# Optimization experiments

Measured on AMD Instinct MI355X. Metric: run time of the kernel, lower is better.

Reference implementation:

```python
import jax, jax.numpy as jnp
import numpy as np

B, D_IN, D_EMB = 8192, 256, 128
N_EX, N_DUR = 16384, 64
N_TRAIN = 100000
THRESH = 1.0


def setup_inputs() -> dict:
    key = jax.random.key(0)
    ks = jax.random.split(key, 6)
    x = jax.random.normal(ks[0], (B, D_IN), jnp.float32)
    # small scales so pairwise distances straddle the threshold (realistic kernel regime)
    W = jax.random.normal(ks[1], (D_IN, D_EMB), jnp.float32) * 0.003
    b = jnp.zeros((D_EMB,), jnp.float32)
    E = jax.random.normal(ks[2], (N_EX, D_EMB), jnp.float32) * 0.05
    log_ev = jax.random.normal(ks[3], (N_EX, N_DUR), jnp.float32)
    log_cen = jax.random.normal(ks[4], (N_EX, N_DUR), jnp.float32)
    logit_h = jax.random.normal(ks[5], (N_DUR,), jnp.float32) - 3.0
    return {
        "input": x, "W": W, "b": b, "exemplar_embeddings": E,
        "log_exemplar_event_counts": log_ev,
        "log_exemplar_censor_counts": log_cen,
        "logit_baseline_hazard": logit_h,
    }


def _kernel_weights(x, W, b, E):
    # encoder (no_grad in original): single linear layer
    phi = x @ W + b  # [B, D_EMB]
    # cdist via Gram expansion; clamp tiny negatives from roundoff
    d2 = (jnp.sum(phi * phi, axis=1, keepdims=True)
          + jnp.sum(E * E, axis=1)[None, :]
          - 2.0 * (phi @ E.T))
    d2 = jnp.maximum(d2, 0.0)          # [B, N_EX] squared distances
    d = jnp.sqrt(d2)
    # threshold mask + exp kernel (matches exp(-distance**2))
    return jnp.where(d <= THRESH, jnp.exp(-d2), 0.0)


def reference(input, W, b, exemplar_embeddings,
              log_exemplar_event_counts, log_exemplar_censor_counts,
              logit_baseline_hazard):
    kw = jax.lax.stop_gradient(
        _kernel_weights(input, W, b, exemplar_embeddings))  # [B, N_EX]

    baseline_hazard = jax.nn.sigmoid(logit_baseline_hazard)  # [N_DUR]
    baseline_KM = jnp.exp(jnp.cumsum(jnp.log(1.0 - baseline_hazard + 1e-7)))

    ev = jnp.exp(log_exemplar_event_counts)    # [N_EX, N_DUR]
    cen = jnp.exp(log_exemplar_censor_counts)  # [N_EX, N_DUR]
    # reverse cumulative sum along durations = flip/cumsum/flip
    at_risk = jnp.flip(jnp.cumsum(jnp.flip(ev + cen, axis=1), axis=1), axis=1)
    pos = at_risk > 0
    hazards = jnp.where(pos, ev / jnp.where(pos, at_risk, 1.0), 0.0)
    exemplar_KM = jnp.exp(jnp.cumsum(jnp.log(1.0 - hazards + 1e-7), axis=1))

    gamma_n = jnp.exp(-(THRESH ** 2)) / N_TRAIN
    numer = kw @ exemplar_KM + gamma_n * baseline_KM[None, :]  # [B, N_DUR]
    denom = (jnp.sum(kw, axis=1) + gamma_n + 1e-12)[:, None]
    return jnp.clip(numer / denom, 1e-12, 1.0 - 1e-12)
```

## Files before the change

### kernel.cpp

```cpp
#include <hip/hip_runtime.h>

using short8  = __attribute__((ext_vector_type(8))) short;
using floatx4 = __attribute__((ext_vector_type(4))) float;

#define NB   8192
#define DIN  256
#define DE   128
#define NEX  16384
#define ND   64
#define ESPLIT 16
#define EPB  (NEX/ESPLIT)
#define TE   64
#define NTIL (EPB/TE)
#define GAMMA_N 3.6787944117144233e-06f

__device__ __forceinline__ unsigned short f2bf(float f) {
  unsigned int u = __float_as_uint(f);
  u += 0x7fffu + ((u >> 16) & 1u);
  return (unsigned short)(u >> 16);
}
__device__ __forceinline__ float bf2f(unsigned short h) {
  return __uint_as_float(((unsigned int)h) << 16);
}

__device__ __forceinline__ void gload_lds16(const void* g, void* l) {
  __builtin_amdgcn_global_load_lds(
      (const __attribute__((address_space(1))) void*)g,
      (__attribute__((address_space(3))) void*)l, 16, 0, 0);
}

__device__ __forceinline__ floatx4 mfma_bf16(short8 a, short8 b, floatx4 c) {
  return __builtin_amdgcn_mfma_f32_16x16x32_bf16(a, b, c, 0, 0, 0);
}

__global__ __launch_bounds__(256) void k_encoder(
    const float* __restrict__ x, const float* __restrict__ W,
    const float* __restrict__ bias, unsigned short* __restrict__ phi_bf,
    float* __restrict__ pn)
{
  __shared__ float xs[32 * DIN];
  __shared__ float part[32][2];
  const int rb  = blockIdx.x * 32;
  const int tid = threadIdx.x;
  for (int i = tid; i < 32 * DIN; i += 256) xs[i] = x[rb * DIN + i];
  __syncthreads();
  const int j  = tid & 127;
  const int rh = tid >> 7;
  const float bj = bias[j];
  float acc[16];
  #pragma unroll
  for (int r = 0; r < 16; ++r) acc[r] = bj;
  for (int k = 0; k < DIN; ++k) {
    const float wv = W[k * DE + j];
    #pragma unroll
    for (int r = 0; r < 16; ++r)
      acc[r] = fmaf(xs[(rh * 16 + r) * DIN + k], wv, acc[r]);
  }
  const int lane = tid & 63;
  const int jh   = (tid >> 6) & 1;
  #pragma unroll
  for (int r = 0; r < 16; ++r) {
    const int row = rh * 16 + r;
    const unsigned short hb = f2bf(acc[r]);
    phi_bf[(rb + row) * DE + j] = hb;
    const float hf = bf2f(hb);
    float sq = hf * hf;
    #pragma unroll
    for (int off = 1; off < 64; off <<= 1) sq += __shfl_xor(sq, off, 64);
    if (lane == 0) part[row][jh] = sq;
  }
  __syncthreads();
  if (tid < 32) pn[rb + tid] = part[tid][0] + part[tid][1];
}

__global__ __launch_bounds__(128) void k_prep_e(
    const float* __restrict__ E, unsigned short* __restrict__ E_bf,
    float* __restrict__ en)
{
  __shared__ float part[2];
  const int e = blockIdx.x;
  const int j = threadIdx.x;
  const unsigned short hb = f2bf(E[e * DE + j]);
  E_bf[e * DE + j] = hb;
  const float hf = bf2f(hb);
  float sq = hf * hf;
  #pragma unroll
  for (int off = 1; off < 64; off <<= 1) sq += __shfl_xor(sq, off, 64);
  if ((j & 63) == 0) part[j >> 6] = sq;
  __syncthreads();
  if (j == 0) en[e] = part[0] + part[1];
}

__global__ __launch_bounds__(256) void k_prep_km(
    const float* __restrict__ lev, const float* __restrict__ lcen,
    const float* __restrict__ lh, unsigned short* __restrict__ KM_t,
    float* __restrict__ baseKM)
{
  __shared__ unsigned short sm[64][65];
  const int tid = threadIdx.x;
  const int t   = tid & 63;
  const int wv  = tid >> 6;
  for (int ee = 0; ee < 16; ++ee) {
    const int el = wv * 16 + ee;
    const int e  = blockIdx.x * 64 + el;
    const float ev = __expf(lev[e * ND + t]);
    const float cn = __expf(lcen[e * ND + t]);
    float s = ev + cn;
    #pragma unroll
    for (int off = 1; off < 64; off <<= 1) {
      const float o = __shfl(s, (t + off) & 63, 64);
      s += (t + off < 64) ? o : 0.0f;
    }
    const float haz = (s > 0.0f) ? (ev / s) : 0.0f;
    float lc = __logf(1.0f - haz + 1e-7f);
    #pragma unroll
    for (int off = 1; off < 64; off <<= 1) {
      const float o = __shfl(lc, (t - off) & 63, 64);
      lc += (t >= off) ? o : 0.0f;
    }
    sm[el][t] = f2bf(__expf(lc));
  }
  __syncthreads();
  const int t_out = tid >> 2, prt = tid & 3;
  unsigned short tmp[16];
  #pragma unroll
  for (int i = 0; i < 16; ++i) tmp[i] = sm[prt * 16 + i][t_out];
  *reinterpret_cast<short8*>(KM_t + (size_t)t_out * NEX + blockIdx.x * 64 + prt * 16) =
      *reinterpret_cast<short8*>(&tmp[0]);
  *reinterpret_cast<short8*>(KM_t + (size_t)t_out * NEX + blockIdx.x * 64 + prt * 16 + 8) =
      *reinterpret_cast<short8*>(&tmp[8]);
  if (blockIdx.x == 0 && tid < 64) {
    const float h = 1.0f / (1.0f + __expf(-lh[t]));
    float l2 = __logf(1.0f - h + 1e-7f);
    #pragma unroll
    for (int off = 1; off < 64; off <<= 1) {
      const float o = __shfl(l2, (t - off) & 63, 64);
      l2 += (t >= off) ? o : 0.0f;
    }
    baseKM[t] = __expf(l2);
  }
}

__global__ __launch_bounds__(256, 4) void k_fused(
    const unsigned short* __restrict__ phi_bf, const float* __restrict__ pn,
    const unsigned short* __restrict__ E_bf, const float* __restrict__ en,
    const unsigned short* __restrict__ KM_t,
    float* __restrict__ numer_p, float* __restrict__ denom_p)
{
  __shared__ __align__(16) unsigned char E_lds[16384];
  __shared__ __align__(16) unsigned char KM_lds[8192];
  __shared__ __align__(16) unsigned char kw_lds[16384];

  const int tid = threadIdx.x;
  const int w   = tid >> 6;
  const int l   = tid & 63;
  const int lr  = l & 15;
  const int g   = l >> 4;
  const int rowbase = blockIdx.y * 128 + w * 32;
  const int ebase0  = blockIdx.x * EPB;
  const int swz = (lr & 7) << 4;

  short8 phiB[2][4];
  float  pnf[2];
  #pragma unroll
  for (int n = 0; n < 2; ++n) {
    const int r = rowbase + n * 16 + lr;
    #pragma unroll
    for (int kq = 0; kq < 4; ++kq)
      phiB[n][kq] = *reinterpret_cast<const short8*>(phi_bf + r * DE + kq * 32 + g * 8);
    pnf[n] = pn[r];
  }

  floatx4 c2[4][2];
  #pragma unroll
  for (int m2 = 0; m2 < 4; ++m2)
    #pragma unroll
    for (int n = 0; n < 2; ++n) c2[m2][n] = (floatx4){0.f, 0.f, 0.f, 0.f};
  float dn[2] = {0.f, 0.f};

  for (int it = 0; it < NTIL; ++it) {
    const int ebase = ebase0 + it * TE;
    __syncthreads();
    #pragma unroll
    for (int i = 0; i < 4; ++i) {
      const int c    = w * 4 + i;
      const int row  = c * 4 + (l >> 4);
      const int colB = (l & 15) * 16;
      gload_lds16((const char*)E_bf + (size_t)(ebase + row) * 256 +
                      (colB ^ ((row & 7) << 4)),
                  &E_lds[c * 1024]);
    }
    #pragma unroll
    for (int i = 0; i < 2; ++i) {
      const int c    = w * 2 + i;
      const int trow = c * 8 + (l >> 3);
      const int colB = (l & 7) * 16;
      gload_lds16((const char*)KM_t + (size_t)trow * (NEX * 2) + ebase * 2 +
                      (colB ^ ((trow & 7) << 4)),
                  &KM_lds[c * 1024]);
    }
    __syncthreads();

    #pragma unroll
    for (int m = 0; m < 4; ++m) {
      short8 ea[4];
      #pragma unroll
      for (int kq = 0; kq < 4; ++kq)
        ea[kq] = *reinterpret_cast<const short8*>(
            &E_lds[(m * 16 + lr) * 256 + ((kq * 64 + g * 16) ^ swz)]);
      floatx4 c1[2];
      c1[0] = (floatx4){0.f, 0.f, 0.f, 0.f};
      c1[1] = (floatx4){0.f, 0.f, 0.f, 0.f};
      #pragma unroll
      for (int kq = 0; kq < 4; ++kq) {
        c1[0] = mfma_bf16(ea[kq], phiB[0][kq], c1[0]);
        c1[1] = mfma_bf16(ea[kq], phiB[1][kq], c1[1]);
      }
      const floatx4 en4 = *reinterpret_cast<const floatx4*>(&en[ebase + m * 16 + g * 4]);
      #pragma unroll
      for (int n = 0; n < 2; ++n) {
        float kwv[4];
        #pragma unroll
        for (int rg = 0; rg < 4; ++rg) {
          float d2 = en4[rg] + pnf[n] - 2.0f * c1[n][rg];
          d2 = fmaxf(d2, 0.0f);
          kwv[rg] = (d2 <= 1.0f) ? __expf(-d2) : 0.0f;
          dn[n] += kwv[rg];
        }
        unsigned int pk0, pk1;
        asm("v_cvt_pk_bf16_f32 %0, %1, %2" : "=v"(pk0) : "v"(kwv[0]), "v"(kwv[1]));
        asm("v_cvt_pk_bf16_f32 %0, %1, %2" : "=v"(pk1) : "v"(kwv[2]), "v"(kwv[3]));
        const unsigned long long pk = (unsigned long long)pk0 |
                                      ((unsigned long long)pk1 << 32);
        *reinterpret_cast<unsigned long long*>(
            &kw_lds[w * 4096 + (n * 16 + lr) * 128 + ((m * 32 + g * 8) ^ swz)]) = pk;
      }
    }

    #pragma unroll
    for (int ks = 0; ks < 2; ++ks) {
      short8 kwB[2];
      #pragma unroll
      for (int n = 0; n < 2; ++n)
        kwB[n] = *reinterpret_cast<const short8*>(
            &kw_lds[w * 4096 + (n * 16 + lr) * 128 + ((ks * 64 + g * 16) ^ swz)]);
      #pragma unroll
      for (int m2 = 0; m2 < 4; ++m2) {
        const short8 kma = *reinterpret_cast<const short8*>(
            &KM_lds[(m2 * 16 + lr) * 128 + ((ks * 64 + g * 16) ^ swz)]);
        c2[m2][0] = mfma_bf16(kma, kwB[0], c2[m2][0]);
        c2[m2][1] = mfma_bf16(kma, kwB[1], c2[m2][1]);
      }
    }
  }

  #pragma unroll
  for (int n = 0; n < 2; ++n) {
    float v = dn[n];
    v += __shfl_xor(v, 16, 64);
    v += __shfl_xor(v, 32, 64);
    if (l < 16) denom_p[(size_t)blockIdx.x * NB + rowbase + n * 16 + lr] = v;
  }
  float* np = numer_p + ((size_t)blockIdx.x * NB + rowbase) * ND;
  #pragma unroll
  for (int n = 0; n < 2; ++n)
    #pragma unroll
    for (int m2 = 0; m2 < 4; ++m2)
      *reinterpret_cast<floatx4*>(&np[(n * 16 + lr) * ND + m2 * 16 + g * 4]) =
          c2[m2][n];
}

__global__ __launch_bounds__(256) void k_finalize(
    const float* __restrict__ numer_p, const float* __restrict__ denom_p,
    const float* __restrict__ baseKM, float* __restrict__ out)
{
  const int idx = blockIdx.x * 256 + threadIdx.x;
  const int b = idx >> 6;
  const int t = idx & 63;
  float num = 0.f, den = 0.f;
  #pragma unroll
  for (int s = 0; s < ESPLIT; ++s) {
    num += numer_p[(size_t)s * NB * ND + idx];
    den += denom_p[(size_t)s * NB + b];
  }
  num += GAMMA_N * baseKM[t];
  den += GAMMA_N + 1e-12f;
  float r = num / den;
  r = fminf(fmaxf(r, 1e-12f), 1.0f - 1e-12f);
  out[idx] = r;
}

extern "C" void kernel_launch(void* const* d_in, const int* in_sizes, int n_in,
                              void* d_out, int out_size, void* d_ws, size_t ws_size,
                              hipStream_t stream)
{
  const float* x    = (const float*)d_in[0];
  const float* W    = (const float*)d_in[1];
  const float* bias = (const float*)d_in[2];
  const float* E    = (const float*)d_in[3];
  const float* lev  = (const float*)d_in[4];
  const float* lcen = (const float*)d_in[5];
  const float* lh   = (const float*)d_in[6];
  float* out = (float*)d_out;

  char* ws = (char*)d_ws;
  size_t off = 0;
  auto alloc = [&](size_t bytes) -> void* {
    void* p = ws + off;
    off += (bytes + 255) & ~(size_t)255;
    return p;
  };
  unsigned short* phi_bf = (unsigned short*)alloc((size_t)NB * DE * 2);
  unsigned short* E_bf   = (unsigned short*)alloc((size_t)NEX * DE * 2);
  unsigned short* KM_t   = (unsigned short*)alloc((size_t)ND * NEX * 2);
  float* pn      = (float*)alloc((size_t)NB * 4);
  float* en      = (float*)alloc((size_t)NEX * 4);
  float* baseKM  = (float*)alloc((size_t)ND * 4);
  float* numer_p = (float*)alloc((size_t)ESPLIT * NB * ND * 4);
  float* denom_p = (float*)alloc((size_t)ESPLIT * NB * 4);

  k_encoder<<<NB / 32, 256, 0, stream>>>(x, W, bias, phi_bf, pn);
  k_prep_e<<<NEX, 128, 0, stream>>>(E, E_bf, en);
  k_prep_km<<<NEX / 64, 256, 0, stream>>>(lev, lcen, lh, KM_t, baseKM);
  k_fused<<<dim3(ESPLIT, NB / 128), 256, 0, stream>>>(phi_bf, pn, E_bf, en, KM_t,
                                                      numer_p, denom_p);
  k_finalize<<<(NB * ND) / 256, 256, 0, stream>>>(numer_p, denom_p, baseKM, out);
}
```

Baseline: 201.3 us.

## Vectorize prep kernels, halve kw LDS tile, store bf16 partials, double E split

```diff
diff --git a/kernel.cpp b/kernel.cpp
--- a/kernel.cpp
+++ b/kernel.cpp
@@ -8,7 +8,7 @@
 #define DE   128
 #define NEX  16384
 #define ND   64
-#define ESPLIT 16
+#define ESPLIT 32
 #define EPB  (NEX/ESPLIT)
 #define TE   64
 #define NTIL (EPB/TE)
@@ -22,6 +22,11 @@
 __device__ __forceinline__ float bf2f(unsigned short h) {
   return __uint_as_float(((unsigned int)h) << 16);
 }
+__device__ __forceinline__ unsigned int pk_bf16(float a, float b) {
+  unsigned int r;
+  asm("v_cvt_pk_bf16_f32 %0, %1, %2" : "=v"(r) : "v"(a), "v"(b));
+  return r;
+}
 
 __device__ __forceinline__ void gload_lds16(const void* g, void* l) {
   __builtin_amdgcn_global_load_lds(
@@ -39,56 +44,78 @@
     float* __restrict__ pn)
 {
   __shared__ float xs[32 * DIN];
-  __shared__ float part[32][2];
   const int rb  = blockIdx.x * 32;
   const int tid = threadIdx.x;
-  for (int i = tid; i < 32 * DIN; i += 256) xs[i] = x[rb * DIN + i];
+  for (int i = tid; i < 32 * DIN / 4; i += 256)
+    reinterpret_cast<float4*>(xs)[i] =
+        reinterpret_cast<const float4*>(x + (size_t)rb * DIN)[i];
   __syncthreads();
-  const int j  = tid & 127;
-  const int rh = tid >> 7;
-  const float bj = bias[j];
-  float acc[16];
-  #pragma unroll
-  for (int r = 0; r < 16; ++r) acc[r] = bj;
+  const int jt = tid & 31;
+  const int rt = tid >> 5;
+  const float4 bj = *reinterpret_cast<const float4*>(&bias[jt * 4]);
+  float4 a0 = bj, a1 = bj, a2 = bj, a3 = bj;
+  const float* xr = xs + rt * 4 * DIN;
+  #pragma unroll 4
   for (int k = 0; k < DIN; ++k) {
-    const float wv = W[k * DE + j];
-    #pragma unroll
-    for (int r = 0; r < 16; ++r)
-      acc[r] = fmaf(xs[(rh * 16 + r) * DIN + k], wv, acc[r]);
-  }
-  const int lane = tid & 63;
-  const int jh   = (tid >> 6) & 1;
-  #pragma unroll
-  for (int r = 0; r < 16; ++r) {
-    const int row = rh * 16 + r;
-    const unsigned short hb = f2bf(acc[r]);
-    phi_bf[(rb + row) * DE + j] = hb;
-    const float hf = bf2f(hb);
-    float sq = hf * hf;
-    #pragma unroll
-    for (int off = 1; off < 64; off <<= 1) sq += __shfl_xor(sq, off, 64);
-    if (lane == 0) part[row][jh] = sq;
-  }
-  __syncthreads();
-  if (tid < 32) pn[rb + tid] = part[tid][0] + part[tid][1];
-}
-
-__global__ __launch_bounds__(128) void k_prep_e(
+    const float4 wv = *reinterpret_cast<const float4*>(&W[k * DE + jt * 4]);
+    const float x0 = xr[k], x1 = xr[DIN + k], x2 = xr[2 * DIN + k], x3 = xr[3 * DIN + k];
+    a0.x = fmaf(x0, wv.x, a0.x); a0.y = fmaf(x0, wv.y, a0.y);
+    a0.z = fmaf(x0, wv.z, a0.z); a0.w = fmaf(x0, wv.w, a0.w);
+    a1.x = fmaf(x1, wv.x, a1.x); a1.y = fmaf(x1, wv.y, a1.y);
+    a1.z = fmaf(x1, wv.z, a1.z); a1.w = fmaf(x1, wv.w, a1.w);
+    a2.x = fmaf(x2, wv.x, a2.x); a2.y = fmaf(x2, wv.y, a2.y);
+    a2.z = fmaf(x2, wv.z, a2.z); a2.w = fmaf(x2, wv.w, a2.w);
+    a3.x = fmaf(x3, wv.x, a3.x); a3.y = fmaf(x3, wv.y, a3.y);
+    a3.z = fmaf(x3, wv.z, a3.z); a3.w = fmaf(x3, wv.w, a3.w);
+  }
+  float4 av[4] = {a0, a1, a2, a3};
+  #pragma unroll
+  for (int rr = 0; rr < 4; ++rr) {
+    const int row = rb + rt * 4 + rr;
+    const unsigned int p0 = pk_bf16(av[rr].x, av[rr].y);
+    const unsigned int p1 = pk_bf16(av[rr].z, av[rr].w);
+    *reinterpret_cast<uint2*>(phi_bf + (size_t)row * DE + jt * 4) =
+        make_uint2(p0, p1);
+    const float h0 = bf2f(p0 & 0xffff), h1 = bf2f(p0 >> 16);
+    const float h2 = bf2f(p1 & 0xffff), h3 = bf2f(p1 >> 16);
+    float s = h0 * h0 + h1 * h1 + h2 * h2 + h3 * h3;
+    s += __shfl_xor(s, 1, 64);
+    s += __shfl_xor(s, 2, 64);
+    s += __shfl_xor(s, 4, 64);
+    s += __shfl_xor(s, 8, 64);
+    s += __shfl_xor(s, 16, 64);
+    if (jt == 0) pn[row] = s;
+  }
+}
+
+__global__ __launch_bounds__(256) void k_prep_e(
     const float* __restrict__ E, unsigned short* __restrict__ E_bf,
     float* __restrict__ en)
 {
-  __shared__ float part[2];
-  const int e = blockIdx.x;
-  const int j = threadIdx.x;
-  const unsigned short hb = f2bf(E[e * DE + j]);
-  E_bf[e * DE + j] = hb;
-  const float hf = bf2f(hb);
-  float sq = hf * hf;
-  #pragma unroll
-  for (int off = 1; off < 64; off <<= 1) sq += __shfl_xor(sq, off, 64);
-  if ((j & 63) == 0) part[j >> 6] = sq;
-  __syncthreads();
-  if (j == 0) en[e] = part[0] + part[1];
+  const int tid = threadIdx.x;
+  const int w = tid >> 6, l = tid & 63;
+  const int row = blockIdx.x * 32 + w * 8 + (l >> 3);
+  const int c0  = (l & 7) * 16;
+  const float4* src = reinterpret_cast<const float4*>(E + (size_t)row * DE + c0);
+  float4 v0 = src[0], v1 = src[1], v2 = src[2], v3 = src[3];
+  unsigned int p[8];
+  p[0] = pk_bf16(v0.x, v0.y); p[1] = pk_bf16(v0.z, v0.w);
+  p[2] = pk_bf16(v1.x, v1.y); p[3] = pk_bf16(v1.z, v1.w);
+  p[4] = pk_bf16(v2.x, v2.y); p[5] = pk_bf16(v2.z, v2.w);
+  p[6] = pk_bf16(v3.x, v3.y); p[7] = pk_bf16(v3.z, v3.w);
+  uint4* dst = reinterpret_cast<uint4*>(E_bf + (size_t)row * DE + c0);
+  dst[0] = make_uint4(p[0], p[1], p[2], p[3]);
+  dst[1] = make_uint4(p[4], p[5], p[6], p[7]);
+  float s = 0.f;
+  #pragma unroll
+  for (int i = 0; i < 8; ++i) {
+    const float lo = bf2f(p[i] & 0xffff), hi = bf2f(p[i] >> 16);
+    s = fmaf(lo, lo, s); s = fmaf(hi, hi, s);
+  }
+  s += __shfl_xor(s, 1, 64);
+  s += __shfl_xor(s, 2, 64);
+  s += __shfl_xor(s, 4, 64);
+  if ((l & 7) == 0) en[row] = s;
 }
 
 __global__ __launch_bounds__(256) void k_prep_km(
@@ -141,15 +168,15 @@
   }
 }
 
-__global__ __launch_bounds__(256, 4) void k_fused(
+__global__ __launch_bounds__(256, 5) void k_fused(
     const unsigned short* __restrict__ phi_bf, const float* __restrict__ pn,
     const unsigned short* __restrict__ E_bf, const float* __restrict__ en,
     const unsigned short* __restrict__ KM_t,
-    float* __restrict__ numer_p, float* __restrict__ denom_p)
+    unsigned short* __restrict__ numer_p, float* __restrict__ denom_p)
 {
   __shared__ __align__(16) unsigned char E_lds[16384];
   __shared__ __align__(16) unsigned char KM_lds[8192];
-  __shared__ __align__(16) unsigned char kw_lds[16384];
+  __shared__ __align__(16) unsigned char kw_lds[8192];
 
   const int tid = threadIdx.x;
   const int w   = tid >> 6;
@@ -158,7 +185,8 @@
   const int g   = l >> 4;
   const int rowbase = blockIdx.y * 128 + w * 32;
   const int ebase0  = blockIdx.x * EPB;
-  const int swz = (lr & 7) << 4;
+  const int swz  = (lr & 7) << 4;
+  const int swz2 = ((lr >> 1) & 3) << 4;
 
   short8 phiB[2][4];
   float  pnf[2];
@@ -202,52 +230,50 @@
     __syncthreads();
 
     #pragma unroll
-    for (int m = 0; m < 4; ++m) {
-      short8 ea[4];
+    for (int h = 0; h < 2; ++h) {
       #pragma unroll
-      for (int kq = 0; kq < 4; ++kq)
-        ea[kq] = *reinterpret_cast<const short8*>(
-            &E_lds[(m * 16 + lr) * 256 + ((kq * 64 + g * 16) ^ swz)]);
-      floatx4 c1[2];
-      c1[0] = (floatx4){0.f, 0.f, 0.f, 0.f};
-      c1[1] = (floatx4){0.f, 0.f, 0.f, 0.f};
-      #pragma unroll
-      for (int kq = 0; kq < 4; ++kq) {
-        c1[0] = mfma_bf16(ea[kq], phiB[0][kq], c1[0]);
-        c1[1] = mfma_bf16(ea[kq], phiB[1][kq], c1[1]);
+      for (int mm = 0; mm < 2; ++mm) {
+        const int m = 2 * h + mm;
+        short8 ea[4];
+        #pragma unroll
+        for (int kq = 0; kq < 4; ++kq)
+          ea[kq] = *reinterpret_cast<const short8*>(
+              &E_lds[(m * 16 + lr) * 256 + ((kq * 64 + g * 16) ^ swz)]);
+        floatx4 c1[2];
+        c1[0] = (floatx4){0.f, 0.f, 0.f, 0.f};
+        c1[1] = (floatx4){0.f, 0.f, 0.f, 0.f};
+        #pragma unroll
+        for (int kq = 0; kq < 4; ++kq) {
+          c1[0] = mfma_bf16(ea[kq], phiB[0][kq], c1[0]);
+          c1[1] = mfma_bf16(ea[kq], phiB[1][kq], c1[1]);
+        }
+        const floatx4 en4 = *reinterpret_cast<const floatx4*>(&en[ebase + m * 16 + g * 4]);
+        #pragma unroll
+        for (int n = 0; n < 2; ++n) {
+          float kwv[4];
+          #pragma unroll
+          for (int rg = 0; rg < 4; ++rg) {
+            const float d2 = en4[rg] + pnf[n] - 2.0f * c1[n][rg];
+            kwv[rg] = (d2 <= 1.0f) ? __expf(-d2) : 0.0f;
+            dn[n] += kwv[rg];
+          }
+          const unsigned int pk0 = pk_bf16(kwv[0], kwv[1]);
+          const unsigned int pk1 = pk_bf16(kwv[2], kwv[3]);
+          const unsigned long long pk = (unsigned long long)pk0 |
+                                        ((unsigned long long)pk1 << 32);
+          *reinterpret_cast<unsigned long long*>(
+              &kw_lds[w * 2048 + (n * 16 + lr) * 64 + ((mm * 32 + g * 8) ^ swz2)]) = pk;
+        }
       }
-      const floatx4 en4 = *reinterpret_cast<const floatx4*>(&en[ebase + m * 16 + g * 4]);
-      #pragma unroll
-      for (int n = 0; n < 2; ++n) {
-        float kwv[4];
-        #pragma unroll
-        for (int rg = 0; rg < 4; ++rg) {
-          float d2 = en4[rg] + pnf[n] - 2.0f * c1[n][rg];
-          d2 = fmaxf(d2, 0.0f);
-          kwv[rg] = (d2 <= 1.0f) ? __expf(-d2) : 0.0f;
-          dn[n] += kwv[rg];
-        }
-        unsigned int pk0, pk1;
-        asm("v_cvt_pk_bf16_f32 %0, %1, %2" : "=v"(pk0) : "v"(kwv[0]), "v"(kwv[1]));
-        asm("v_cvt_pk_bf16_f32 %0, %1, %2" : "=v"(pk1) : "v"(kwv[2]), "v"(kwv[3]));
-        const unsigned long long pk = (unsigned long long)pk0 |
-                                      ((unsigned long long)pk1 << 32);
-        *reinterpret_cast<unsigned long long*>(
-            &kw_lds[w * 4096 + (n * 16 + lr) * 128 + ((m * 32 + g * 8) ^ swz)]) = pk;
-      }
-    }
-
-    #pragma unroll
-    for (int ks = 0; ks < 2; ++ks) {
       short8 kwB[2];
       #pragma unroll
       for (int n = 0; n < 2; ++n)
         kwB[n] = *reinterpret_cast<const short8*>(
-            &kw_lds[w * 4096 + (n * 16 + lr) * 128 + ((ks * 64 + g * 16) ^ swz)]);
+            &kw_lds[w * 2048 + (n * 16 + lr) * 64 + ((g * 16) ^ swz2)]);
       #pragma unroll
       for (int m2 = 0; m2 < 4; ++m2) {
         const short8 kma = *reinterpret_cast<const short8*>(
-            &KM_lds[(m2 * 16 + lr) * 128 + ((ks * 64 + g * 16) ^ swz)]);
+            &KM_lds[(m2 * 16 + lr) * 128 + ((h * 64 + g * 16) ^ swz)]);
         c2[m2][0] = mfma_bf16(kma, kwB[0], c2[m2][0]);
         c2[m2][1] = mfma_bf16(kma, kwB[1], c2[m2][1]);
       }
@@ -261,17 +287,21 @@
     v += __shfl_xor(v, 32, 64);
     if (l < 16) denom_p[(size_t)blockIdx.x * NB + rowbase + n * 16 + lr] = v;
   }
-  float* np = numer_p + ((size_t)blockIdx.x * NB + rowbase) * ND;
-  #pragma unroll
-  for (int n = 0; n < 2; ++n)
-    #pragma unroll
-    for (int m2 = 0; m2 < 4; ++m2)
-      *reinterpret_cast<floatx4*>(&np[(n * 16 + lr) * ND + m2 * 16 + g * 4]) =
-          c2[m2][n];
+  #pragma unroll
+  for (int n = 0; n < 2; ++n) {
+    const size_t rowoff = ((size_t)blockIdx.x * NB + rowbase + n * 16 + lr) * ND;
+    #pragma unroll
+    for (int m2 = 0; m2 < 4; ++m2) {
+      const unsigned int q0 = pk_bf16(c2[m2][n][0], c2[m2][n][1]);
+      const unsigned int q1 = pk_bf16(c2[m2][n][2], c2[m2][n][3]);
+      *reinterpret_cast<uint2*>(numer_p + rowoff + m2 * 16 + g * 4) =
+          make_uint2(q0, q1);
+    }
+  }
 }
 
 __global__ __launch_bounds__(256) void k_finalize(
-    const float* __restrict__ numer_p, const float* __restrict__ denom_p,
+    const unsigned short* __restrict__ numer_p, const float* __restrict__ denom_p,
     const float* __restrict__ baseKM, float* __restrict__ out)
 {
   const int idx = blockIdx.x * 256 + threadIdx.x;
@@ -280,7 +310,7 @@
   float num = 0.f, den = 0.f;
   #pragma unroll
   for (int s = 0; s < ESPLIT; ++s) {
-    num += numer_p[(size_t)s * NB * ND + idx];
+    num += bf2f(numer_p[(size_t)s * NB * ND + idx]);
     den += denom_p[(size_t)s * NB + b];
   }
   num += GAMMA_N * baseKM[t];
@@ -310,17 +340,17 @@
     off += (bytes + 255) & ~(size_t)255;
     return p;
   };
-  unsigned short* phi_bf = (unsigned short*)alloc((size_t)NB * DE * 2);
-  unsigned short* E_bf   = (unsigned short*)alloc((size_t)NEX * DE * 2);
-  unsigned short* KM_t   = (unsigned short*)alloc((size_t)ND * NEX * 2);
-  float* pn      = (float*)alloc((size_t)NB * 4);
-  float* en      = (float*)alloc((size_t)NEX * 4);
-  float* baseKM  = (float*)alloc((size_t)ND * 4);
-  float* numer_p = (float*)alloc((size_t)ESPLIT * NB * ND * 4);
-  float* denom_p = (float*)alloc((size_t)ESPLIT * NB * 4);
+  unsigned short* phi_bf  = (unsigned short*)alloc((size_t)NB * DE * 2);
+  unsigned short* E_bf    = (unsigned short*)alloc((size_t)NEX * DE * 2);
+  unsigned short* KM_t    = (unsigned short*)alloc((size_t)ND * NEX * 2);
+  float* pn       = (float*)alloc((size_t)NB * 4);
+  float* en       = (float*)alloc((size_t)NEX * 4);
+  float* baseKM   = (float*)alloc((size_t)ND * 4);
+  unsigned short* numer_p = (unsigned short*)alloc((size_t)ESPLIT * NB * ND * 2);
+  float* denom_p  = (float*)alloc((size_t)ESPLIT * NB * 4);
 
   k_encoder<<<NB / 32, 256, 0, stream>>>(x, W, bias, phi_bf, pn);
-  k_prep_e<<<NEX, 128, 0, stream>>>(E, E_bf, en);
+  k_prep_e<<<NEX / 32, 256, 0, stream>>>(E, E_bf, en);
   k_prep_km<<<NEX / 64, 256, 0, stream>>>(lev, lcen, lh, KM_t, baseKM);
   k_fused<<<dim3(ESPLIT, NB / 128), 256, 0, stream>>>(phi_bf, pn, E_bf, en, KM_t,
                                                       numer_p, denom_p);
```

Result: slower. 302.7 us (+50.4%).
